# Kernel optimization log

Measured on AMD Instinct MI355X. Metric: run time of the kernel, lower is better.

The kernel has to match this reference:

```python
import jax, jax.numpy as jnp
import numpy as np

EMBED = 1024
HEADS = 16
HEAD_DIM = EMBED // HEADS
HIDDEN = 4 * EMBED
EPS = 1e-5


def layer_norm(x, g, b):
    mu = jnp.mean(x, axis=-1, keepdims=True)
    var = jnp.var(x, axis=-1, keepdims=True)
    return (x - mu) * jax.lax.rsqrt(var + EPS) * g + b


def setup_inputs() -> dict:
    key = jax.random.key(0)
    ks = jax.random.split(key, 12)
    s_e = 1.0 / np.sqrt(EMBED)
    s_h = 1.0 / np.sqrt(HIDDEN)
    return {
        "x": jax.random.normal(ks[0], (8, 1024, EMBED), dtype=jnp.float32),
        "ln1_g": jnp.ones((EMBED,), jnp.float32),
        "ln1_b": jnp.zeros((EMBED,), jnp.float32),
        "w_qkv": jax.random.normal(ks[1], (EMBED, 3 * EMBED), jnp.float32) * s_e,
        "b_qkv": jax.random.normal(ks[2], (3 * EMBED,), jnp.float32) * s_e,
        "w_out": jax.random.normal(ks[3], (EMBED, EMBED), jnp.float32) * s_e,
        "b_out": jax.random.normal(ks[4], (EMBED,), jnp.float32) * s_e,
        "ln2_g": jnp.ones((EMBED,), jnp.float32),
        "ln2_b": jnp.zeros((EMBED,), jnp.float32),
        "w_up": jax.random.normal(ks[5], (EMBED, HIDDEN), jnp.float32) * s_e,
        "b_up": jax.random.normal(ks[6], (HIDDEN,), jnp.float32) * s_e,
        "w_down": jax.random.normal(ks[7], (HIDDEN, EMBED), jnp.float32) * s_h,
        "b_down": jax.random.normal(ks[8], (EMBED,), jnp.float32) * s_h,
    }


def reference(x, ln1_g, ln1_b, w_qkv, b_qkv, w_out, b_out,
              ln2_g, ln2_b, w_up, b_up, w_down, b_down):
    B, T, C = x.shape
    # --- attention sub-block ---
    h = layer_norm(x, ln1_g, ln1_b)
    qkv = h @ w_qkv + b_qkv                                   # [B,T,3C]
    q, k, v = jnp.split(qkv, 3, axis=-1)
    def heads(t):  # [B,T,C] -> [B,H,T,D]
        return t.reshape(B, T, HEADS, HEAD_DIM).transpose(0, 2, 1, 3)
    q, k, v = heads(q), heads(k), heads(v)
    scale = HEAD_DIM ** -0.5
    attn = jax.nn.softmax(jnp.einsum('bhqd,bhkd->bhqk', q, k) * scale, axis=-1)
    y = jnp.einsum('bhqk,bhkd->bhqd', attn, v)                # [B,H,T,D]
    y = y.transpose(0, 2, 1, 3).reshape(B, T, C)
    x = x + y @ w_out + b_out
    # --- MLP sub-block ---
    h = layer_norm(x, ln2_g, ln2_b)
    h = jax.nn.relu(h @ w_up + b_up)
    x = x + h @ w_down + b_down
    return x
```

## Files before the change

### kernel.cpp

```cpp
#include <hip/hip_runtime.h>
#include <stdint.h>


typedef __attribute__((ext_vector_type(8))) short short8;
typedef __attribute__((ext_vector_type(4))) short short4v;
typedef __attribute__((ext_vector_type(4))) float floatx4;

#define NROWS 8192

__device__ __forceinline__ unsigned short f2bf(float f) {
    union { float f; unsigned u; } x; x.f = f;
    unsigned r = x.u + 0x7fffu + ((x.u >> 16) & 1u);
    return (unsigned short)(r >> 16);
}
__device__ __forceinline__ float bf2f(unsigned short h) {
    union { unsigned u; float f; } x; x.u = (unsigned)h << 16; return x.f;
}

__device__ __forceinline__ void gl2lds16(const unsigned short* g, unsigned short* l) {
    __builtin_amdgcn_global_load_lds(
        (const __attribute__((address_space(1))) unsigned int*)(uintptr_t)g,
        (__attribute__((address_space(3))) unsigned int*)(unsigned int)(uintptr_t)l,
        16, 0, 0);
}

__global__ __launch_bounds__(256) void prep_kernel(
    const float* __restrict__ w_qkv, const float* __restrict__ w_out,
    const float* __restrict__ w_up, const float* __restrict__ w_down,
    unsigned short* __restrict__ wqkvT, unsigned short* __restrict__ woutT,
    unsigned short* __restrict__ wupT, unsigned short* __restrict__ wdownT,
    const float* __restrict__ x, const float* __restrict__ g,
    const float* __restrict__ b, unsigned short* __restrict__ h1)
{
    int bid = blockIdx.x;
    __shared__ unsigned short tile[32][33];
    __shared__ float rs[4], rs2[4];
    if (bid < 12288) {
        const float* in; unsigned short* out; int K, N, nb, tb;
        if (bid < 3072)      { in = w_qkv;  out = wqkvT;  K = 1024; N = 3072; nb = 96;  tb = bid; }
        else if (bid < 4096) { in = w_out;  out = woutT;  K = 1024; N = 1024; nb = 32;  tb = bid - 3072; }
        else if (bid < 8192) { in = w_up;   out = wupT;   K = 1024; N = 4096; nb = 128; tb = bid - 4096; }
        else                 { in = w_down; out = wdownT; K = 4096; N = 1024; nb = 32;  tb = bid - 8192; }
        int n0 = (tb % nb) * 32, k0 = (tb / nb) * 32;
        int tx = threadIdx.x & 31, ty = threadIdx.x >> 5;
        #pragma unroll
        for (int i = 0; i < 4; ++i)
            tile[ty + i * 8][tx] = f2bf(in[(size_t)(k0 + ty + i * 8) * N + n0 + tx]);
        __syncthreads();
        #pragma unroll
        for (int i = 0; i < 4; ++i)
            out[(size_t)(n0 + ty + i * 8) * K + k0 + tx] = tile[tx][ty + i * 8];
    } else {
        int row = bid - 12288, t = threadIdx.x;
        const float4* xr = (const float4*)(x + (size_t)row * 1024);
        float4 v = xr[t];
        float s  = v.x + v.y + v.z + v.w;
        float s2 = v.x * v.x + v.y * v.y + v.z * v.z + v.w * v.w;
        #pragma unroll
        for (int off = 32; off; off >>= 1) {
            s  += __shfl_xor(s,  off, 64);
            s2 += __shfl_xor(s2, off, 64);
        }
        int w = t >> 6;
        if ((t & 63) == 0) { rs[w] = s; rs2[w] = s2; }
        __syncthreads();
        s  = rs[0] + rs[1] + rs[2] + rs[3];
        s2 = rs2[0] + rs2[1] + rs2[2] + rs2[3];
        float mean = s * (1.0f / 1024.0f);
        float var  = s2 * (1.0f / 1024.0f) - mean * mean;
        float rstd = rsqrtf(var + 1e-5f);
        float4 gv = ((const float4*)g)[t];
        float4 bv = ((const float4*)b)[t];
        ushort4 o;
        o.x = f2bf((v.x - mean) * rstd * gv.x + bv.x);
        o.y = f2bf((v.y - mean) * rstd * gv.y + bv.y);
        o.z = f2bf((v.z - mean) * rstd * gv.z + bv.z);
        o.w = f2bf((v.w - mean) * rstd * gv.w + bv.w);
        ((ushort4*)(h1 + (size_t)row * 1024))[t] = o;
    }
}

__global__ __launch_bounds__(256) void ln_bf16b(
    const unsigned short* __restrict__ x, const float* __restrict__ g,
    const float* __restrict__ b, unsigned short* __restrict__ out)
{
    int row = blockIdx.x, t = threadIdx.x;
    ushort4 hv = ((const ushort4*)(x + (size_t)row * 1024))[t];
    float v0 = bf2f(hv.x), v1 = bf2f(hv.y), v2 = bf2f(hv.z), v3 = bf2f(hv.w);
    float s  = v0 + v1 + v2 + v3;
    float s2 = v0 * v0 + v1 * v1 + v2 * v2 + v3 * v3;
    #pragma unroll
    for (int off = 32; off; off >>= 1) {
        s  += __shfl_xor(s,  off, 64);
        s2 += __shfl_xor(s2, off, 64);
    }
    __shared__ float rs[4], rs2[4];
    int w = t >> 6;
    if ((t & 63) == 0) { rs[w] = s; rs2[w] = s2; }
    __syncthreads();
    s  = rs[0] + rs[1] + rs[2] + rs[3];
    s2 = rs2[0] + rs2[1] + rs2[2] + rs2[3];
    float mean = s * (1.0f / 1024.0f);
    float var  = s2 * (1.0f / 1024.0f) - mean * mean;
    float rstd = rsqrtf(var + 1e-5f);
    float4 gv = ((const float4*)g)[t];
    float4 bv = ((const float4*)b)[t];
    ushort4 o;
    o.x = f2bf((v0 - mean) * rstd * gv.x + bv.x);
    o.y = f2bf((v1 - mean) * rstd * gv.y + bv.y);
    o.z = f2bf((v2 - mean) * rstd * gv.z + bv.z);
    o.w = f2bf((v3 - mean) * rstd * gv.w + bv.w);
    ((ushort4*)(out + (size_t)row * 1024))[t] = o;
}

template <int MODE>
__global__ __launch_bounds__(256, 3) void gemm_db128(
    const unsigned short* __restrict__ A, const unsigned short* __restrict__ Bt,
    int M, int N, int K,
    const float* __restrict__ bias,
    unsigned short* __restrict__ outB,
    unsigned short* __restrict__ qO, unsigned short* __restrict__ kO,
    unsigned short* __restrict__ vO)
{
    int m0 = blockIdx.x * 128, n0 = blockIdx.y * 128;
    int tid = threadIdx.x;
    int w = tid >> 6, l = tid & 63, quad = l >> 4, lr = l & 15;
    int wm = w & 1, wn = w >> 1;

    __shared__ unsigned short S[2][256 * 32];

    floatx4 acc[4][4];
    #pragma unroll
    for (int i = 0; i < 4; ++i)
        #pragma unroll
        for (int j = 0; j < 4; ++j)
            acc[i][j] = (floatx4){0.f, 0.f, 0.f, 0.f};

    int srow = l >> 2;
    int scol = ((l & 3) ^ (srow & 3)) * 8;
    const unsigned short* gp[4];
    int lofs[4];
    #pragma unroll
    for (int u = 0; u < 4; ++u) {
        int rb = 64 * w + 16 * u;
        if (rb < 128) gp[u] = A  + (size_t)(m0 + rb + srow) * K + scol;
        else          gp[u] = Bt + (size_t)(n0 + rb - 128 + srow) * K + scol;
        lofs[u] = rb * 32;
    }

    #pragma unroll
    for (int u = 0; u < 4; ++u) gl2lds16(gp[u], &S[0][lofs[u]]);
    __syncthreads();

    for (int kt = 0; kt < K; kt += 32) {
        int cur = (kt >> 5) & 1;
        if (kt + 32 < K) {
            #pragma unroll
            for (int u = 0; u < 4; ++u)
                gl2lds16(gp[u] + kt + 32, &S[cur ^ 1][lofs[u]]);
        }
        short8 af[4], bf[4];
        #pragma unroll
        for (int i = 0; i < 4; ++i)
            af[i] = *(const short8*)
                &S[cur][(64 * wm + 16 * i + lr) * 32 + ((quad ^ (lr & 3)) * 8)];
        #pragma unroll
        for (int j = 0; j < 4; ++j)
            bf[j] = *(const short8*)
                &S[cur][(128 + 64 * wn + 16 * j + lr) * 32 + ((quad ^ (lr & 3)) * 8)];
        #pragma unroll
        for (int i = 0; i < 4; ++i)
            #pragma unroll
            for (int j = 0; j < 4; ++j)
                acc[i][j] = __builtin_amdgcn_mfma_f32_16x16x32_bf16(
                    af[i], bf[j], acc[i][j], 0, 0, 0);
        __syncthreads();
    }

    if (MODE == 0) {
        int sel = n0 >> 10;
        if (sel < 2) {
            const float qscale = (sel == 0) ? 0.125f : 1.0f;
            unsigned short* dst = (sel == 0) ? qO : kO;
            #pragma unroll
            for (int i = 0; i < 4; ++i)
                #pragma unroll
                for (int j = 0; j < 4; ++j)
                    #pragma unroll
                    for (int r = 0; r < 4; ++r) {
                        int m = m0 + 64 * wm + 16 * i + quad * 4 + r;
                        int n = n0 + 64 * wn + 16 * j + lr;
                        float c = (acc[i][j][r] + bias[n]) * qscale;
                        int bb = m >> 10, t = m & 1023;
                        int cc = n & 1023, h = cc >> 6, d = cc & 63;
                        dst[(((size_t)(bb * 16 + h)) * 1024 + t) * 64 + d] = f2bf(c);
                    }
        } else {
            int bb = m0 >> 10;
            #pragma unroll
            for (int i = 0; i < 4; ++i) {
                int t0 = (m0 & 1023) + 64 * wm + 16 * i + quad * 4;
                #pragma unroll
                for (int j = 0; j < 4; ++j) {
                    int n = n0 + 64 * wn + 16 * j + lr;
                    int cc = n & 1023, h = cc >> 6, d = cc & 63;
                    float bn = bias[n];
                    ushort4 pk;
                    pk.x = f2bf(acc[i][j][0] + bn);
                    pk.y = f2bf(acc[i][j][1] + bn);
                    pk.z = f2bf(acc[i][j][2] + bn);
                    pk.w = f2bf(acc[i][j][3] + bn);
                    *(ushort4*)&vO[((size_t)(bb * 16 + h) * 64 + d) * 1024 + t0] = pk;
                }
            }
        }
    } else {
        #pragma unroll
        for (int i = 0; i < 4; ++i)
            #pragma unroll
            for (int j = 0; j < 4; ++j)
                #pragma unroll
                for (int r = 0; r < 4; ++r) {
                    int m = m0 + 64 * wm + 16 * i + quad * 4 + r;
                    int n = n0 + 64 * wn + 16 * j + lr;
                    outB[(size_t)m * N + n] = f2bf(fmaxf(acc[i][j][r] + bias[n], 0.f));
                }
    }
}

template <int MODE>
__global__ __launch_bounds__(256, 2) void gemm_dbuf(
    const unsigned short* __restrict__ A, const unsigned short* __restrict__ Bt,
    int M, int N, int K,
    const float* __restrict__ bias,
    const float* __restrict__ residF, const unsigned short* __restrict__ residB,
    float* __restrict__ outF, unsigned short* __restrict__ outB)
{
    int m0 = blockIdx.x * 128, n0 = blockIdx.y * 128;
    int tid = threadIdx.x;
    int w = tid >> 6, l = tid & 63, quad = l >> 4, lr = l & 15;
    int wm = w & 1, wn = w >> 1;

    __shared__ unsigned short As[2][128 * 64];
    __shared__ unsigned short Bs[2][128 * 64];

    floatx4 acc[4][4];
    #pragma unroll
    for (int i = 0; i < 4; ++i)
        #pragma unroll
        for (int j = 0; j < 4; ++j)
            acc[i][j] = (floatx4){0.f, 0.f, 0.f, 0.f};

    int srow = l >> 3;
    int scol = ((l & 7) ^ srow) * 8;
    const unsigned short* Ag = A  + (size_t)(m0 + 32 * w + srow) * K + scol;
    const unsigned short* Bg = Bt + (size_t)(n0 + 32 * w + srow) * K + scol;

    #pragma unroll
    for (int u = 0; u < 4; ++u) {
        gl2lds16(Ag + (size_t)(8 * u) * K, &As[0][(32 * w + 8 * u) * 64]);
        gl2lds16(Bg + (size_t)(8 * u) * K, &Bs[0][(32 * w + 8 * u) * 64]);
    }
    __syncthreads();

    for (int kt = 0; kt < K; kt += 64) {
        int cur = (kt >> 6) & 1;
        if (kt + 64 < K) {
            #pragma unroll
            for (int u = 0; u < 4; ++u) {
                gl2lds16(Ag + (size_t)(8 * u) * K + kt + 64,
                         &As[cur ^ 1][(32 * w + 8 * u) * 64]);
                gl2lds16(Bg + (size_t)(8 * u) * K + kt + 64,
                         &Bs[cur ^ 1][(32 * w + 8 * u) * 64]);
            }
        }
        short8 af[4][2], bf[4][2];
        #pragma unroll
        for (int i = 0; i < 4; ++i)
            #pragma unroll
            for (int s = 0; s < 2; ++s)
                af[i][s] = *(const short8*)
                    &As[cur][(64 * wm + 16 * i + lr) * 64 + (((s * 4 + quad) ^ (lr & 7)) * 8)];
        #pragma unroll
        for (int j = 0; j < 4; ++j)
            #pragma unroll
            for (int s = 0; s < 2; ++s)
                bf[j][s] = *(const short8*)
                    &Bs[cur][(64 * wn + 16 * j + lr) * 64 + (((s * 4 + quad) ^ (lr & 7)) * 8)];
        #pragma unroll
        for (int i = 0; i < 4; ++i)
            #pragma unroll
            for (int j = 0; j < 4; ++j) {
                acc[i][j] = __builtin_amdgcn_mfma_f32_16x16x32_bf16(
                    af[i][0], bf[j][0], acc[i][j], 0, 0, 0);
                acc[i][j] = __builtin_amdgcn_mfma_f32_16x16x32_bf16(
                    af[i][1], bf[j][1], acc[i][j], 0, 0, 0);
            }
        __syncthreads();
    }

    #pragma unroll
    for (int i = 0; i < 4; ++i)
        #pragma unroll
        for (int j = 0; j < 4; ++j)
            #pragma unroll
            for (int r = 0; r < 4; ++r) {
                int m = m0 + 64 * wm + 16 * i + quad * 4 + r;
                int n = n0 + 64 * wn + 16 * j + lr;
                float c = acc[i][j][r] + bias[n];
                if (MODE == 1)
                    outB[(size_t)m * N + n] = f2bf(c + residF[(size_t)m * N + n]);
                else
                    outF[(size_t)m * N + n] = c + bf2f(residB[(size_t)m * N + n]);
            }
}

__global__ __launch_bounds__(256, 2) void attn_kernel(
    const unsigned short* __restrict__ qg, const unsigned short* __restrict__ kg,
    const unsigned short* __restrict__ vtg, unsigned short* __restrict__ y)
{
    int bid = blockIdx.x;
    int bh = bid & 127, qt = bid >> 7;
    int b = bh >> 4, h = bh & 15;
    int tid = threadIdx.x;
    int w = tid >> 6, l = tid & 63, quad = l >> 4, lr = l & 15;

    __shared__ unsigned short Qs[128 * 64];
    __shared__ unsigned short Ks[2][64 * 64];
    __shared__ unsigned short Vs[2][64 * 64];
    __shared__ unsigned short Ps[4][32 * 68];

    int srow = l >> 3;
    int scol = ((l & 7) ^ srow) * 8;

    {
        const unsigned short* qbase = qg + (size_t)bh * 65536 + (size_t)(qt * 128) * 64;
        #pragma unroll
        for (int u = 0; u < 4; ++u)
            gl2lds16(qbase + (size_t)(32 * w + 8 * u + srow) * 64 + scol,
                     &Qs[(32 * w + 8 * u) * 64]);
    }
    const unsigned short* kbase = kg  + (size_t)bh * 65536;
    const unsigned short* vbase = vtg + (size_t)bh * 65536;

    #pragma unroll
    for (int u = 0; u < 2; ++u) {
        gl2lds16(kbase + (size_t)(16 * w + 8 * u + srow) * 64 + scol,
                 &Ks[0][(16 * w + 8 * u) * 64]);
        gl2lds16(vbase + (size_t)(16 * w + 8 * u + srow) * 1024 + scol,
                 &Vs[0][(16 * w + 8 * u) * 64]);
    }
    __syncthreads();

    short8 af[2][2];
    #pragma unroll
    for (int i = 0; i < 2; ++i)
        #pragma unroll
        for (int s = 0; s < 2; ++s)
            af[i][s] = *(const short8*)
                &Qs[(32 * w + 16 * i + lr) * 64 + ((s * 4 + quad) ^ (lr & 7)) * 8];

    floatx4 o[2][4];
    float lsum[2][4];
    #pragma unroll
    for (int i = 0; i < 2; ++i)
        #pragma unroll
        for (int j = 0; j < 4; ++j) o[i][j] = (floatx4){0.f, 0.f, 0.f, 0.f};
    #pragma unroll
    for (int i = 0; i < 2; ++i)
        #pragma unroll
        for (int r = 0; r < 4; ++r) lsum[i][r] = 0.f;

    for (int kt = 0; kt < 16; ++kt) {
        int cur = kt & 1;
        if (kt + 1 < 16) {
            const unsigned short* kb = kbase + (size_t)((kt + 1) * 64) * 64;
            const unsigned short* vb = vbase + (size_t)((kt + 1) * 64);
            #pragma unroll
            for (int u = 0; u < 2; ++u) {
                gl2lds16(kb + (size_t)(16 * w + 8 * u + srow) * 64 + scol,
                         &Ks[cur ^ 1][(16 * w + 8 * u) * 64]);
                gl2lds16(vb + (size_t)(16 * w + 8 * u + srow) * 1024 + scol,
                         &Vs[cur ^ 1][(16 * w + 8 * u) * 64]);
            }
        }

        short8 kf[4][2];
        #pragma unroll
        for (int j = 0; j < 4; ++j)
            #pragma unroll
            for (int s = 0; s < 2; ++s)
                kf[j][s] = *(const short8*)
                    &Ks[cur][(16 * j + lr) * 64 + ((s * 4 + quad) ^ (lr & 7)) * 8];

        floatx4 s[2][4];
        #pragma unroll
        for (int i = 0; i < 2; ++i)
            #pragma unroll
            for (int j = 0; j < 4; ++j) {
                s[i][j] = (floatx4){0.f, 0.f, 0.f, 0.f};
                #pragma unroll
                for (int st = 0; st < 2; ++st)
                    s[i][j] = __builtin_amdgcn_mfma_f32_16x16x32_bf16(
                        af[i][st], kf[j][st], s[i][j], 0, 0, 0);
            }

        #pragma unroll
        for (int i = 0; i < 2; ++i)
            #pragma unroll
            for (int j = 0; j < 4; ++j)
                #pragma unroll
                for (int r = 0; r < 4; ++r) {
                    float p = __expf(s[i][j][r]);
                    lsum[i][r] += p;
                    Ps[w][(16 * i + quad * 4 + r) * 68 + 16 * j + lr] = f2bf(p);
                }

        asm volatile("s_waitcnt lgkmcnt(0)" ::: "memory");

        short8 vf[4][2];
        #pragma unroll
        for (int j = 0; j < 4; ++j)
            #pragma unroll
            for (int s = 0; s < 2; ++s)
                vf[j][s] = *(const short8*)
                    &Vs[cur][(16 * j + lr) * 64 + ((s * 4 + quad) ^ (lr & 7)) * 8];

        #pragma unroll
        for (int i = 0; i < 2; ++i)
            #pragma unroll
            for (int st = 0; st < 2; ++st) {
                short4v p0 = *(const short4v*)&Ps[w][(16 * i + lr) * 68 + st * 32 + quad * 8];
                short4v p1 = *(const short4v*)&Ps[w][(16 * i + lr) * 68 + st * 32 + quad * 8 + 4];
                short8 pf;
                #pragma unroll
                for (int e = 0; e < 4; ++e) { pf[e] = p0[e]; pf[e + 4] = p1[e]; }
                #pragma unroll
                for (int j = 0; j < 4; ++j)
                    o[i][j] = __builtin_amdgcn_mfma_f32_16x16x32_bf16(
                        pf, vf[j][st], o[i][j], 0, 0, 0);
            }
        __syncthreads();
    }

    #pragma unroll
    for (int off = 8; off; off >>= 1)
        #pragma unroll
        for (int i = 0; i < 2; ++i)
            #pragma unroll
            for (int r = 0; r < 4; ++r)
                lsum[i][r] += __shfl_xor(lsum[i][r], off, 64);
    float rinv[2][4];
    #pragma unroll
    for (int i = 0; i < 2; ++i)
        #pragma unroll
        for (int r = 0; r < 4; ++r) rinv[i][r] = 1.0f / lsum[i][r];

    #pragma unroll
    for (int i = 0; i < 2; ++i)
        #pragma unroll
        for (int j = 0; j < 4; ++j)
            #pragma unroll
            for (int r = 0; r < 4; ++r) {
                int trow = qt * 128 + 32 * w + 16 * i + quad * 4 + r;
                int col  = h * 64 + 16 * j + lr;
                y[((size_t)b * 1024 + trow) * 1024 + col] =
                    f2bf(o[i][j][r] * rinv[i][r]);
            }
}

extern "C" void kernel_launch(void* const* d_in, const int* in_sizes, int n_in,
                              void* d_out, int out_size, void* d_ws, size_t ws_size,
                              hipStream_t stream)
{
    const float* x      = (const float*)d_in[0];
    const float* ln1_g  = (const float*)d_in[1];
    const float* ln1_b  = (const float*)d_in[2];
    const float* w_qkv  = (const float*)d_in[3];
    const float* b_qkv  = (const float*)d_in[4];
    const float* w_out  = (const float*)d_in[5];
    const float* b_out  = (const float*)d_in[6];
    const float* ln2_g  = (const float*)d_in[7];
    const float* ln2_b  = (const float*)d_in[8];
    const float* w_up   = (const float*)d_in[9];
    const float* b_up   = (const float*)d_in[10];
    const float* w_down = (const float*)d_in[11];
    const float* b_down = (const float*)d_in[12];

    char* ws = (char*)d_ws;
    unsigned short* wqkvT  = (unsigned short*)(ws + 0);
    unsigned short* woutT  = (unsigned short*)(ws + 6291456);
    unsigned short* wupT   = (unsigned short*)(ws + 8388608);
    unsigned short* wdownT = (unsigned short*)(ws + 16777216);
    unsigned short* x2     = (unsigned short*)(ws + 25165824);
    unsigned short* h1     = (unsigned short*)(ws + 58720256);
    unsigned short* qb     = (unsigned short*)(ws + 75497472);
    unsigned short* kb     = (unsigned short*)(ws + 92274688);
    unsigned short* vtb    = (unsigned short*)(ws + 109051904);
    unsigned short* yb     = (unsigned short*)(ws + 125829120);
    unsigned short* a2     = (unsigned short*)(ws + 75497472);
    unsigned short* h2     = h1;

    prep_kernel<<<20480, 256, 0, stream>>>(
        w_qkv, w_out, w_up, w_down, wqkvT, woutT, wupT, wdownT,
        x, ln1_g, ln1_b, h1);

    gemm_db128<0><<<dim3(NROWS / 128, 3072 / 128), 256, 0, stream>>>(
        h1, wqkvT, NROWS, 3072, 1024, b_qkv, nullptr, qb, kb, vtb);

    attn_kernel<<<1024, 256, 0, stream>>>(qb, kb, vtb, yb);

    gemm_dbuf<1><<<dim3(NROWS / 128, 1024 / 128), 256, 0, stream>>>(
        yb, woutT, NROWS, 1024, 1024, b_out, x, nullptr, nullptr, x2);

    ln_bf16b<<<NROWS, 256, 0, stream>>>(x2, ln2_g, ln2_b, h2);

    gemm_db128<2><<<dim3(NROWS / 128, 4096 / 128), 256, 0, stream>>>(
        h2, wupT, NROWS, 4096, 1024, b_up, a2, nullptr, nullptr, nullptr);

    gemm_dbuf<3><<<dim3(NROWS / 128, 1024 / 128), 256, 0, stream>>>(
        a2, wdownT, NROWS, 1024, 4096, b_down, nullptr, x2, (float*)d_out, nullptr);
}
```

Baseline: 464.0 us.

## Replace 128x128 GEMM with 256x256 eight-wave phased-pipeline kernel for QKV and up-proj

Replaces the 128x128-tile, 4-wave double-buffered bf16 GEMM used for the QKV and MLP up-projection with a 256x256-tile, 8-wave kernel. It uses K-step 64 with separate swizzled A/B LDS buffers and issues global-to-LDS loads in four phases interleaved with MFMA work. Explicit vmcnt waits, raw barriers and s_setprio overlap loads with compute. The larger tile raises arithmetic intensity and cuts global traffic, at the cost of more registers and 128KB of LDS. The fewer, larger blocks could also hurt occupancy or wave balance.

```diff
diff --git a/kernel.cpp b/kernel.cpp
--- a/kernel.cpp
+++ b/kernel.cpp
@@ -114,7 +114,7 @@
 }
 
 template <int MODE>
-__global__ __launch_bounds__(256, 3) void gemm_db128(
+__global__ __launch_bounds__(512, 2) void gemm_8ph(
     const unsigned short* __restrict__ A, const unsigned short* __restrict__ Bt,
     int M, int N, int K,
     const float* __restrict__ bias,
@@ -122,108 +122,150 @@
     unsigned short* __restrict__ qO, unsigned short* __restrict__ kO,
     unsigned short* __restrict__ vO)
 {
-    int m0 = blockIdx.x * 128, n0 = blockIdx.y * 128;
+    int m0 = blockIdx.x * 256, n0 = blockIdx.y * 256;
     int tid = threadIdx.x;
     int w = tid >> 6, l = tid & 63, quad = l >> 4, lr = l & 15;
-    int wm = w & 1, wn = w >> 1;
-
-    __shared__ unsigned short S[2][256 * 32];
-
-    floatx4 acc[4][4];
-    #pragma unroll
-    for (int i = 0; i < 4; ++i)
+    int wm = w >> 2, wn = w & 3;
+
+    __shared__ unsigned short As[2][256 * 64];
+    __shared__ unsigned short Bs[2][256 * 64];
+
+    floatx4 acc[8][4];
+    #pragma unroll
+    for (int i = 0; i < 8; ++i)
         #pragma unroll
         for (int j = 0; j < 4; ++j)
             acc[i][j] = (floatx4){0.f, 0.f, 0.f, 0.f};
 
-    int srow = l >> 2;
-    int scol = ((l & 3) ^ (srow & 3)) * 8;
-    const unsigned short* gp[4];
-    int lofs[4];
-    #pragma unroll
-    for (int u = 0; u < 4; ++u) {
-        int rb = 64 * w + 16 * u;
-        if (rb < 128) gp[u] = A  + (size_t)(m0 + rb + srow) * K + scol;
-        else          gp[u] = Bt + (size_t)(n0 + rb - 128 + srow) * K + scol;
-        lofs[u] = rb * 32;
-    }
-
-    #pragma unroll
-    for (int u = 0; u < 4; ++u) gl2lds16(gp[u], &S[0][lofs[u]]);
-    __syncthreads();
-
-    for (int kt = 0; kt < K; kt += 32) {
-        int cur = (kt >> 5) & 1;
-        if (kt + 32 < K) {
-            #pragma unroll
-            for (int u = 0; u < 4; ++u)
-                gl2lds16(gp[u] + kt + 32, &S[cur ^ 1][lofs[u]]);
+    int srow = l >> 3;
+    int swz  = ((l & 7) ^ srow) * 8;
+    int arow1 = (w < 4) ? 16 * w : 128 + 16 * (w - 4);
+    const unsigned short* Ag = A  + (size_t)(m0 + arow1 + srow) * K + swz;
+    const unsigned short* Bg = Bt + (size_t)(n0 + 16 * w + srow) * K + swz;
+    int nt = K >> 6;
+
+    auto SB = [&](unsigned short* dst, int h, int kt) {
+        #pragma unroll
+        for (int u = 0; u < 2; ++u)
+            gl2lds16(Bg + (size_t)(128 * h + 8 * u) * K + kt * 64,
+                     &dst[(128 * h + 16 * w + 8 * u) * 64]);
+    };
+    auto SA1 = [&](unsigned short* dst, int kt) {
+        #pragma unroll
+        for (int u = 0; u < 2; ++u)
+            gl2lds16(Ag + (size_t)(8 * u) * K + kt * 64,
+                     &dst[(arow1 + 8 * u) * 64]);
+    };
+    auto SA2 = [&](unsigned short* dst, int kt) {
+        #pragma unroll
+        for (int u = 0; u < 2; ++u)
+            gl2lds16(Ag + (size_t)(64 + 8 * u) * K + kt * 64,
+                     &dst[(arow1 + 64 + 8 * u) * 64]);
+    };
+
+    SB(Bs[0], 0, 0); SB(Bs[0], 1, 0); SA1(As[0], 0); SA2(As[0], 0);
+    SB(Bs[1], 0, 1); SB(Bs[1], 1, 1); SA1(As[1], 1);
+    asm volatile("s_waitcnt vmcnt(6)" ::: "memory");
+    __builtin_amdgcn_s_barrier();
+
+    for (int t = 0; t < nt; ++t) {
+        int b = t & 1;
+        const unsigned short* Asb = As[b];
+        const unsigned short* Bsb = Bs[b];
+        short8 bfr[4][2];
+        #pragma unroll
+        for (int p = 0; p < 4; ++p) {
+            if (p == 0)      { if (t + 1 < nt) SA2(As[b ^ 1], t + 1); }
+            else if (p == 1) { if (t + 2 < nt) SB(Bs[b], 0, t + 2); }
+            else if (p == 2) { if (t + 2 < nt) SB(Bs[b], 1, t + 2); }
+            else             { if (t + 2 < nt) SA1(As[b], t + 2); }
+
+            if (p == 0) {
+                #pragma unroll
+                for (int j = 0; j < 4; ++j)
+                    #pragma unroll
+                    for (int s = 0; s < 2; ++s)
+                        bfr[j][s] = *(const short8*)
+                            &Bsb[(64 * wn + 16 * j + lr) * 64 +
+                                 (((s * 4 + quad) ^ (lr & 7)) * 8)];
+            }
+            short8 af[2][2];
+            #pragma unroll
+            for (int i = 0; i < 2; ++i)
+                #pragma unroll
+                for (int s = 0; s < 2; ++s)
+                    af[i][s] = *(const short8*)
+                        &Asb[(128 * wm + 32 * p + 16 * i + lr) * 64 +
+                             (((s * 4 + quad) ^ (lr & 7)) * 8)];
+
+            __builtin_amdgcn_s_barrier();
+            asm volatile("s_waitcnt lgkmcnt(0)" ::: "memory");
+            __builtin_amdgcn_s_setprio(1);
+            #pragma unroll
+            for (int i = 0; i < 2; ++i)
+                #pragma unroll
+                for (int j = 0; j < 4; ++j) {
+                    acc[2 * p + i][j] = __builtin_amdgcn_mfma_f32_16x16x32_bf16(
+                        af[i][0], bfr[j][0], acc[2 * p + i][j], 0, 0, 0);
+                    acc[2 * p + i][j] = __builtin_amdgcn_mfma_f32_16x16x32_bf16(
+                        af[i][1], bfr[j][1], acc[2 * p + i][j], 0, 0, 0);
+                }
+            __builtin_amdgcn_s_setprio(0);
+            if (p == 3) {
+                if (t + 2 >= nt) asm volatile("s_waitcnt vmcnt(0)" ::: "memory");
+                else             asm volatile("s_waitcnt vmcnt(6)" ::: "memory");
+            }
+            __builtin_amdgcn_s_barrier();
         }
-        short8 af[4], bf[4];
-        #pragma unroll
-        for (int i = 0; i < 4; ++i)
-            af[i] = *(const short8*)
-                &S[cur][(64 * wm + 16 * i + lr) * 32 + ((quad ^ (lr & 3)) * 8)];
-        #pragma unroll
-        for (int j = 0; j < 4; ++j)
-            bf[j] = *(const short8*)
-                &S[cur][(128 + 64 * wn + 16 * j + lr) * 32 + ((quad ^ (lr & 3)) * 8)];
-        #pragma unroll
-        for (int i = 0; i < 4; ++i)
-            #pragma unroll
-            for (int j = 0; j < 4; ++j)
-                acc[i][j] = __builtin_amdgcn_mfma_f32_16x16x32_bf16(
-                    af[i], bf[j], acc[i][j], 0, 0, 0);
-        __syncthreads();
     }
 
     if (MODE == 0) {
-        int sel = n0 >> 10;
+        int sel = (n0 + 64 * wn) >> 10;
         if (sel < 2) {
             const float qscale = (sel == 0) ? 0.125f : 1.0f;
             unsigned short* dst = (sel == 0) ? qO : kO;
             #pragma unroll
-            for (int i = 0; i < 4; ++i)
+            for (int mi = 0; mi < 8; ++mi)
                 #pragma unroll
                 for (int j = 0; j < 4; ++j)
                     #pragma unroll
                     for (int r = 0; r < 4; ++r) {
-                        int m = m0 + 64 * wm + 16 * i + quad * 4 + r;
+                        int m = m0 + 128 * wm + 16 * mi + quad * 4 + r;
                         int n = n0 + 64 * wn + 16 * j + lr;
-                        float c = (acc[i][j][r] + bias[n]) * qscale;
-                        int bb = m >> 10, t = m & 1023;
-                        int cc = n & 1023, h = cc >> 6, d = cc & 63;
-                        dst[(((size_t)(bb * 16 + h)) * 1024 + t) * 64 + d] = f2bf(c);
+                        float c = (acc[mi][j][r] + bias[n]) * qscale;
+                        int bb = m >> 10, tt = m & 1023;
+                        int cc = n & 1023, hh = cc >> 6, d = cc & 63;
+                        dst[(((size_t)(bb * 16 + hh)) * 1024 + tt) * 64 + d] = f2bf(c);
                     }
         } else {
             int bb = m0 >> 10;
             #pragma unroll
-            for (int i = 0; i < 4; ++i) {
-                int t0 = (m0 & 1023) + 64 * wm + 16 * i + quad * 4;
+            for (int mi = 0; mi < 8; ++mi) {
+                int t0 = (m0 & 1023) + 128 * wm + 16 * mi + quad * 4;
                 #pragma unroll
                 for (int j = 0; j < 4; ++j) {
                     int n = n0 + 64 * wn + 16 * j + lr;
-                    int cc = n & 1023, h = cc >> 6, d = cc & 63;
+                    int cc = n & 1023, hh = cc >> 6, d = cc & 63;
                     float bn = bias[n];
                     ushort4 pk;
-                    pk.x = f2bf(acc[i][j][0] + bn);
-                    pk.y = f2bf(acc[i][j][1] + bn);
-                    pk.z = f2bf(acc[i][j][2] + bn);
-                    pk.w = f2bf(acc[i][j][3] + bn);
-                    *(ushort4*)&vO[((size_t)(bb * 16 + h) * 64 + d) * 1024 + t0] = pk;
+                    pk.x = f2bf(acc[mi][j][0] + bn);
+                    pk.y = f2bf(acc[mi][j][1] + bn);
+                    pk.z = f2bf(acc[mi][j][2] + bn);
+                    pk.w = f2bf(acc[mi][j][3] + bn);
+                    *(ushort4*)&vO[((size_t)(bb * 16 + hh) * 64 + d) * 1024 + t0] = pk;
                 }
             }
         }
     } else {
         #pragma unroll
-        for (int i = 0; i < 4; ++i)
+        for (int mi = 0; mi < 8; ++mi)
             #pragma unroll
             for (int j = 0; j < 4; ++j)
                 #pragma unroll
                 for (int r = 0; r < 4; ++r) {
-                    int m = m0 + 64 * wm + 16 * i + quad * 4 + r;
+                    int m = m0 + 128 * wm + 16 * mi + quad * 4 + r;
                     int n = n0 + 64 * wn + 16 * j + lr;
-                    outB[(size_t)m * N + n] = f2bf(fmaxf(acc[i][j][r] + bias[n], 0.f));
+                    outB[(size_t)m * N + n] = f2bf(fmaxf(acc[mi][j][r] + bias[n], 0.f));
                 }
     }
 }
@@ -505,7 +547,7 @@
         w_qkv, w_out, w_up, w_down, wqkvT, woutT, wupT, wdownT,
         x, ln1_g, ln1_b, h1);
 
-    gemm_db128<0><<<dim3(NROWS / 128, 3072 / 128), 256, 0, stream>>>(
+    gemm_8ph<0><<<dim3(NROWS / 256, 3072 / 256), 512, 0, stream>>>(
         h1, wqkvT, NROWS, 3072, 1024, b_qkv, nullptr, qb, kb, vtb);
 
     attn_kernel<<<1024, 256, 0, stream>>>(qb, kb, vtb, yb);
@@ -515,7 +557,7 @@
 
     ln_bf16b<<<NROWS, 256, 0, stream>>>(x2, ln2_g, ln2_b, h2);
 
-    gemm_db128<2><<<dim3(NROWS / 128, 4096 / 128), 256, 0, stream>>>(
+    gemm_8ph<2><<<dim3(NROWS / 256, 4096 / 256), 512, 0, stream>>>(
         h2, wupT, NROWS, 4096, 1024, b_up, a2, nullptr, nullptr, nullptr);
 
     gemm_dbuf<3><<<dim3(NROWS / 128, 1024 / 128), 256, 0, stream>>>(
```

New measurement: 434.7 us. -6.3%, faster.
